# Kernel optimization log

Hardware: AMD Instinct MI355X
Metric: run time of the kernel (lower is better)

The kernel has to match this reference:

```python
import jax, jax.numpy as jnp
import numpy as np

N_NODES = 100000
N_EDGES = 600000
N_GRAPHS = 512
VOCAB = 4096
EMB = 128
HID = 128


def setup_inputs() -> dict:
    key = jax.random.key(0)
    ks = jax.random.split(key, 8)
    x = jax.random.randint(ks[0], (N_NODES,), 0, VOCAB)
    edge_index = jax.random.randint(ks[1], (2, N_EDGES), 0, N_NODES)
    batch = jnp.sort(jax.random.randint(ks[2], (N_NODES,), 0, N_GRAPHS))
    emb = jax.random.normal(ks[3], (VOCAB, EMB), dtype=jnp.float32)
    W1 = jax.random.normal(ks[4], (EMB, HID), dtype=jnp.float32) / np.sqrt(EMB)
    b1 = jnp.zeros((HID,), dtype=jnp.float32)
    W2 = jax.random.normal(ks[5], (HID, HID), dtype=jnp.float32) / np.sqrt(HID)
    b2 = jnp.zeros((HID,), dtype=jnp.float32)
    return {"x": x, "edge_index": edge_index, "batch": batch,
            "emb": emb, "W1": W1, "b1": b1, "W2": W2, "b2": b2}


def gcn_conv(h, src, dst, W, b, n_nodes):
    # PyG GCNConv: linear transform, then symmetric-normalized scatter-sum
    # (self-loops already included in src/dst), plus bias.
    h = h @ W
    deg = jax.ops.segment_sum(jnp.ones(dst.shape, h.dtype), dst, num_segments=n_nodes)
    dis = jnp.where(deg > 0, jax.lax.rsqrt(jnp.maximum(deg, 1.0)), 0.0)
    norm = dis[src] * dis[dst]                      # [E]
    msg = h[src] * norm[:, None]                    # gather + scale
    out = jax.ops.segment_sum(msg, dst, num_segments=n_nodes)
    return out + b


def reference(x, edge_index, batch, emb, W1, b1, W2, b2):
    n = x.shape[0]
    loop = jnp.arange(n)
    src = jnp.concatenate([edge_index[0], loop])    # add self-loops, as GCNConv does
    dst = jnp.concatenate([edge_index[1], loop])

    h = emb[x]                                      # [N, EMB] embedding lookup
    h = jax.nn.relu(gcn_conv(h, src, dst, W1, b1, n))
    # dropout: identity in eval mode
    h = gcn_conv(h, src, dst, W2, b2, n)            # [N, HID]

    # global_mean_pool over graph ids
    sums = jax.ops.segment_sum(h, batch, num_segments=N_GRAPHS)
    cnts = jax.ops.segment_sum(jnp.ones((n,), h.dtype), batch, num_segments=N_GRAPHS)
    return sums / jnp.maximum(cnts, 1.0)[:, None]   # [N_GRAPHS, HID]
```

## Files before the change

### kernel.cpp

```cpp
#include <hip/hip_runtime.h>
#include <hip/hip_bf16.h>
#include <hip/hip_fp16.h>

#define D 128

__device__ __forceinline__ float bf2f(unsigned short u) {
  return __uint_as_float(((unsigned int)u) << 16);
}
__device__ __forceinline__ unsigned short f2bf(float f) {
  unsigned int x = __float_as_uint(f);
  x += 0x7fff + ((x >> 16) & 1);
  return (unsigned short)(x >> 16);
}
__device__ __forceinline__ float h2f(unsigned short b) {
  return __half2float(__ushort_as_half(b));
}


__global__ void k_detect_f5(const unsigned short* __restrict__ t0, int n0,
                            const unsigned short* __restrict__ t1, int n1,
                            const unsigned short* __restrict__ t2, int n2,
                            const unsigned short* __restrict__ t3, int n3,
                            const unsigned short* __restrict__ t4, int n4,
                            int* __restrict__ flag) {
  const unsigned short* tabs[5] = {t0, t1, t2, t3, t4};
  int ns[5] = {n0, n1, n2, n3, n4};
  int b = blockIdx.x;
  const unsigned short* u16 = tabs[b];
  int n = ns[b];
  __shared__ int cnt;
  int K = n / 2 < 256 ? n / 2 : 256;
  if (threadIdx.x == 0) cnt = 0;
  __syncthreads();
  if (threadIdx.x < K) {
    unsigned short u = u16[threadIdx.x * 2];
    int e = (u >> 7) & 0xFF;
    if (u == 0 || (e >= 100 && e <= 140)) atomicAdd(&cnt, 1);
  }
  __syncthreads();
  if (threadIdx.x == 0) flag[b] = (cnt * 2 >= K) ? 1 : 0;
}

__global__ void k_detect_i(const unsigned int* __restrict__ ei32,
                           int* __restrict__ flagSlot) {
  __shared__ int z;
  if (threadIdx.x == 0) z = 0;
  __syncthreads();
  if (ei32[threadIdx.x * 2 + 1] == 0u) atomicAdd(&z, 1);
  __syncthreads();
  if (threadIdx.x == 0) *flagSlot = (z >= 60) ? 1 : 0;
}

__global__ void k_conv(const void* __restrict__ src, float* __restrict__ dst,
                       int n, const int* __restrict__ flagSlot) {
  int i = blockIdx.x * blockDim.x + threadIdx.x;
  if (i >= n) return;
  if (*flagSlot) dst[i] = bf2f(((const unsigned short*)src)[i]);
  else           dst[i] = ((const float*)src)[i];
}

__global__ void k_conv_params(const void* __restrict__ W1, const void* __restrict__ b1,
                              const void* __restrict__ W2, const void* __restrict__ b2,
                              float* __restrict__ W1f, float* __restrict__ b1f,
                              float* __restrict__ W2f, float* __restrict__ b2f,
                              const int* __restrict__ flag) {
  int i = blockIdx.x * blockDim.x + threadIdx.x;
  const int S = D * D;
  const void* src; float* dst; int j; const int* fs;
  if (i < S)                { src = W1; dst = W1f; j = i;            fs = flag + 1; }
  else if (i < S + D)       { src = b1; dst = b1f; j = i - S;        fs = flag + 2; }
  else if (i < 2 * S + D)   { src = W2; dst = W2f; j = i - S - D;    fs = flag + 3; }
  else if (i < 2 * S + 2*D) { src = b2; dst = b2f; j = i - 2*S - D;  fs = flag + 4; }
  else return;
  if (*fs) dst[j] = bf2f(((const unsigned short*)src)[j]);
  else     dst[j] = ((const float*)src)[j];
}

__global__ void k_convi_all(const void* __restrict__ xr, const void* __restrict__ eir,
                            const void* __restrict__ br,
                            int* __restrict__ xs, int* __restrict__ srcs,
                            int* __restrict__ dsts, int* __restrict__ batchs,
                            int* __restrict__ indeg,
                            int nn, int ne, int vocab, int ng,
                            const int* __restrict__ flag64) {
  long long i = (long long)blockIdx.x * blockDim.x + threadIdx.x;
  int is64 = *flag64;
  if (i < nn) {
    int v = is64 ? (int)((const long long*)xr)[i] : ((const int*)xr)[i];
    v = v < 0 ? 0 : (v > vocab - 1 ? vocab - 1 : v);
    xs[i] = v;
  } else if (i < (long long)nn + ne) {
    long long j = i - nn;
    int v = is64 ? (int)((const long long*)eir)[j] : ((const int*)eir)[j];
    v = v < 0 ? 0 : (v > nn - 1 ? nn - 1 : v);
    srcs[j] = v;
  } else if (i < (long long)nn + 2 * ne) {
    long long j = i - nn - ne;
    int v = is64 ? (int)((const long long*)eir)[ne + j] : ((const int*)eir)[ne + j];
    v = v < 0 ? 0 : (v > nn - 1 ? nn - 1 : v);
    dsts[j] = v;
    atomicAdd(&indeg[v], 1);
  } else if (i < 2LL * nn + 2 * ne) {
    long long j = i - nn - 2 * ne;
    int v = is64 ? (int)((const long long*)br)[j] : ((const int*)br)[j];
    v = v < 0 ? 0 : (v > ng - 1 ? ng - 1 : v);
    batchs[j] = v;
  }
}

__global__ __launch_bounds__(1024) void k_scan1(const int* __restrict__ indeg,
                                                int* __restrict__ off,
                                                int* __restrict__ bsum, int nn) {
  int t = threadIdx.x;
  int idx = blockIdx.x * 1024 + t;
  int v = (idx < nn) ? indeg[idx] : 0;
  int lane = t & 63, wid = t >> 6;
  int inc = v;
  #pragma unroll
  for (int d = 1; d < 64; d <<= 1) {
    int u = __shfl_up(inc, d);
    if (lane >= d) inc += u;
  }
  __shared__ int ws[16];
  if (lane == 63) ws[wid] = inc;
  __syncthreads();
  if (wid == 0) {
    int wv = (lane < 16) ? ws[lane] : 0;
    #pragma unroll
    for (int d = 1; d < 16; d <<= 1) {
      int u = __shfl_up(wv, d);
      if (lane >= d) wv += u;
    }
    if (lane < 16) ws[lane] = wv;
  }
  __syncthreads();
  int base = wid ? ws[wid - 1] : 0;
  if (idx < nn) off[idx] = base + inc - v;
  if (t == 1023) bsum[blockIdx.x] = ws[15];
}

__global__ void k_scan2(int* __restrict__ bsum, int nb) {
  if (blockIdx.x == 0 && threadIdx.x == 0) {
    int run = 0;
    for (int i = 0; i < nb; ++i) { int s = bsum[i]; bsum[i] = run; run += s; }
  }
}

__global__ void k_scan3(int* __restrict__ off, int* __restrict__ cursor,
                        float* __restrict__ dis, const int* __restrict__ indeg,
                        const int* __restrict__ bsum, int nn) {
  int idx = blockIdx.x * blockDim.x + threadIdx.x;
  if (idx >= nn) return;
  int o = off[idx] + bsum[idx >> 10];
  off[idx] = o;
  cursor[idx] = o;
  dis[idx] = rsqrtf((float)indeg[idx] + 1.0f);
}

__global__ void k_fill(const int* __restrict__ srcA, const int* __restrict__ dstA,
                       const int* __restrict__ xs, const float* __restrict__ dis,
                       int* __restrict__ cursor, int2* __restrict__ csr, int ne) {
  int e = blockIdx.x * blockDim.x + threadIdx.x;
  if (e >= ne) return;
  int d = dstA[e], s = srcA[e];
  unsigned short hb = __half_as_ushort(__float2half_rn(dis[s]));
  unsigned int packed = (unsigned int)xs[s] | ((unsigned int)hb << 16);
  int pp = atomicAdd(&cursor[d], 1);
  csr[pp] = make_int2(s, (int)packed);
}

__global__ void k_gemm_dumb(const float* __restrict__ A,
                            const float* __restrict__ W,
                            float* __restrict__ OUT, int rows) {
  int idx = blockIdx.x * blockDim.x + threadIdx.x;
  if (idx >= rows * D) return;
  int r = idx >> 7, c = idx & 127;
  const float* a = A + (size_t)r * D;
  float acc = 0.f;
  for (int k = 0; k < D; ++k) acc += a[k] * W[k * D + c];
  OUT[idx] = acc;
}

__global__ __launch_bounds__(256) void k_aggrelu(const int* __restrict__ x,
                                                 const float* __restrict__ G,
                                                 const float* __restrict__ b1,
                                                 const int* __restrict__ off,
                                                 const int* __restrict__ indeg,
                                                 const float* __restrict__ dis,
                                                 const int2* __restrict__ csr,
                                                 unsigned short* __restrict__ H1,
                                                 int nn) {
  int gid = blockIdx.x * blockDim.x + threadIdx.x;
  int n = gid >> 5;
  if (n >= nn) return;
  int lane = threadIdx.x & 31;
  float dn = dis[n];
  float4 g0 = ((const float4*)(G + (size_t)x[n] * D))[lane];
  float ax = dn * g0.x, ay = dn * g0.y, az = dn * g0.z, aw = dn * g0.w;
  int s0 = off[n], m = indeg[n];
  if (m >= 2) {
    unsigned int c0 = (unsigned int)csr[s0].y, c1 = (unsigned int)csr[s0 + 1].y;
    int j = 0;
    for (; j + 3 < m; j += 2) {
      unsigned int p0 = (unsigned int)csr[s0 + j + 2].y;
      unsigned int p1 = (unsigned int)csr[s0 + j + 3].y;
      float w0 = h2f((unsigned short)(c0 >> 16));
      float w1 = h2f((unsigned short)(c1 >> 16));
      float4 gA = ((const float4*)(G + (size_t)(c0 & 0xFFFF) * D))[lane];
      float4 gB = ((const float4*)(G + (size_t)(c1 & 0xFFFF) * D))[lane];
      ax += w0 * gA.x + w1 * gB.x;
      ay += w0 * gA.y + w1 * gB.y;
      az += w0 * gA.z + w1 * gB.z;
      aw += w0 * gA.w + w1 * gB.w;
      c0 = p0; c1 = p1;
    }
    {
      float w0 = h2f((unsigned short)(c0 >> 16));
      float w1 = h2f((unsigned short)(c1 >> 16));
      float4 gA = ((const float4*)(G + (size_t)(c0 & 0xFFFF) * D))[lane];
      float4 gB = ((const float4*)(G + (size_t)(c1 & 0xFFFF) * D))[lane];
      ax += w0 * gA.x + w1 * gB.x;
      ay += w0 * gA.y + w1 * gB.y;
      az += w0 * gA.z + w1 * gB.z;
      aw += w0 * gA.w + w1 * gB.w;
    }
    if (j + 2 < m) {
      unsigned int e0 = (unsigned int)csr[s0 + j + 2].y;
      float w0 = h2f((unsigned short)(e0 >> 16));
      float4 gA = ((const float4*)(G + (size_t)(e0 & 0xFFFF) * D))[lane];
      ax += w0 * gA.x; ay += w0 * gA.y; az += w0 * gA.z; aw += w0 * gA.w;
    }
  } else if (m == 1) {
    unsigned int e0 = (unsigned int)csr[s0].y;
    float w0 = h2f((unsigned short)(e0 >> 16));
    float4 gA = ((const float4*)(G + (size_t)(e0 & 0xFFFF) * D))[lane];
    ax += w0 * gA.x; ay += w0 * gA.y; az += w0 * gA.z; aw += w0 * gA.w;
  }
  float4 bb = ((const float4*)b1)[lane];
  ushort4 o;
  o.x = f2bf(dn * fmaxf(dn * ax + bb.x, 0.f));
  o.y = f2bf(dn * fmaxf(dn * ay + bb.y, 0.f));
  o.z = f2bf(dn * fmaxf(dn * az + bb.z, 0.f));
  o.w = f2bf(dn * fmaxf(dn * aw + bb.w, 0.f));
  ((ushort4*)(H1 + (size_t)n * D))[lane] = o;
}

__global__ __launch_bounds__(256) void k_agg2pool(
    const unsigned short* __restrict__ H1, const int* __restrict__ off,
    const int* __restrict__ indeg, const float* __restrict__ dis,
    const int2* __restrict__ csr, const int* __restrict__ batch,
    float* __restrict__ P, int nn) {
  __shared__ float buf[8][D];
  __shared__ int gbuf[8];
  int t = threadIdx.x;
  int slot = t >> 5, lane = t & 31;
  int n = blockIdx.x * 8 + slot;
  float ax = 0.f, ay = 0.f, az = 0.f, aw = 0.f;
  if (n < nn) {
    float dn = dis[n];
    ushort4 u0 = ((const ushort4*)(H1 + (size_t)n * D))[lane];
    ax = bf2f(u0.x); ay = bf2f(u0.y); az = bf2f(u0.z); aw = bf2f(u0.w);
    int s0 = off[n], m = indeg[n];
    if (m >= 2) {
      int c0 = csr[s0].x, c1 = csr[s0 + 1].x;
      int j = 0;
      for (; j + 3 < m; j += 2) {
        int p0 = csr[s0 + j + 2].x;
        int p1 = csr[s0 + j + 3].x;
        ushort4 hA = ((const ushort4*)(H1 + (size_t)c0 * D))[lane];
        ushort4 hB = ((const ushort4*)(H1 + (size_t)c1 * D))[lane];
        ax += bf2f(hA.x) + bf2f(hB.x);
        ay += bf2f(hA.y) + bf2f(hB.y);
        az += bf2f(hA.z) + bf2f(hB.z);
        aw += bf2f(hA.w) + bf2f(hB.w);
        c0 = p0; c1 = p1;
      }
      {
        ushort4 hA = ((const ushort4*)(H1 + (size_t)c0 * D))[lane];
        ushort4 hB = ((const ushort4*)(H1 + (size_t)c1 * D))[lane];
        ax += bf2f(hA.x) + bf2f(hB.x);
        ay += bf2f(hA.y) + bf2f(hB.y);
        az += bf2f(hA.z) + bf2f(hB.z);
        aw += bf2f(hA.w) + bf2f(hB.w);
      }
      if (j + 2 < m) {
        int e0 = csr[s0 + j + 2].x;
        ushort4 hA = ((const ushort4*)(H1 + (size_t)e0 * D))[lane];
        ax += bf2f(hA.x); ay += bf2f(hA.y); az += bf2f(hA.z); aw += bf2f(hA.w);
      }
    } else if (m == 1) {
      int e0 = csr[s0].x;
      ushort4 hA = ((const ushort4*)(H1 + (size_t)e0 * D))[lane];
      ax += bf2f(hA.x); ay += bf2f(hA.y); az += bf2f(hA.z); aw += bf2f(hA.w);
    }
    ax *= dn; ay *= dn; az *= dn; aw *= dn;
  }
  ((float4*)&buf[slot][lane * 4])[0] = make_float4(ax, ay, az, aw);
  if (lane == 0) gbuf[slot] = (n < nn) ? batch[n] : -1;
  __syncthreads();
  if (t < D) {
    int c = t;
    float acc = 0.f;
    int run = -1;
    #pragma unroll
    for (int s2 = 0; s2 < 8; ++s2) {
      int g = gbuf[s2];
      if (g < 0) break;
      if (g != run) {
        if (run >= 0) atomicAdd(&P[(size_t)run * D + c], acc);
        run = g;
        acc = 0.f;
      }
      acc += buf[s2][c];
    }
    if (run >= 0) atomicAdd(&P[(size_t)run * D + c], acc);
  }
}

__global__ void k_cnt2(const int* __restrict__ batch, int* __restrict__ cnt,
                       int nn, int ng) {
  int g = blockIdx.x * blockDim.x + threadIdx.x;
  if (g >= ng) return;
  int lo = 0, hi = nn;
  while (lo < hi) { int m = (lo + hi) >> 1; if (batch[m] < g) lo = m + 1; else hi = m; }
  int s = lo;
  hi = nn;
  while (lo < hi) { int m = (lo + hi) >> 1; if (batch[m] < g + 1) lo = m + 1; else hi = m; }
  cnt[g] = lo - s;
}

__global__ void k_out_dumb(const float* __restrict__ P,
                           const int* __restrict__ cnt,
                           const float* __restrict__ W2,
                           const float* __restrict__ b2,
                           float* __restrict__ Out, int ng) {
  int idx = blockIdx.x * blockDim.x + threadIdx.x;
  if (idx >= ng * D) return;
  int g = idx >> 7, c = idx & 127;
  int m = cnt[g];
  float inv = (m > 0) ? (1.0f / (float)m) : 0.0f;
  const float* pr = P + (size_t)g * D;
  float acc = 0.f;
  for (int k = 0; k < D; ++k) acc += pr[k] * W2[k * D + c];
  acc *= inv;
  if (m > 0) acc += b2[c];
  Out[idx] = acc;
}

extern "C" void kernel_launch(void* const* d_in, const int* in_sizes, int n_in,
                              void* d_out, int out_size, void* d_ws, size_t ws_size,
                              hipStream_t stream) {
  const void* xr = d_in[0];
  const void* eir = d_in[1];
  const void* batchr = d_in[2];
  const void* emb = d_in[3];
  const void* W1 = d_in[4];
  const void* b1 = d_in[5];
  const void* W2 = d_in[6];
  const void* b2 = d_in[7];
  float* out = (float*)d_out;

  const int nn = in_sizes[0];
  const int ne = in_sizes[1] / 2;
  const int vocab = in_sizes[3] / D;
  const int ng = out_size / D;
  const int nb = (nn + 1023) / 1024;

  char* p = (char*)d_ws;
  auto alloc = [&](size_t bytes) -> char* {
    char* r = p;
    p += (bytes + 511) & ~(size_t)511;
    return r;
  };
  int* flag = (int*)alloc(512);
  int* xs = (int*)alloc((size_t)nn * 4);
  int* srcs = (int*)alloc((size_t)ne * 4);
  int* dsts = (int*)alloc((size_t)ne * 4);
  int* batchs = (int*)alloc((size_t)nn * 4);
  int* indeg = (int*)alloc((size_t)nn * 4);
  int* off = (int*)alloc((size_t)nn * 4);
  int* cursor = (int*)alloc((size_t)nn * 4);
  float* dis = (float*)alloc((size_t)nn * 4);
  int* bsum = (int*)alloc((size_t)nb * 4);
  int* cnt = (int*)alloc((size_t)ng * 4);
  int2* csr = (int2*)alloc((size_t)ne * 8);
  float* embf = (float*)alloc((size_t)vocab * D * 4);
  float* W1f = (float*)alloc((size_t)D * D * 4);
  float* b1f = (float*)alloc((size_t)D * 4);
  float* W2f = (float*)alloc((size_t)D * D * 4);
  float* b2f = (float*)alloc((size_t)D * 4);
  float* G = (float*)alloc((size_t)vocab * D * 4);
  unsigned short* H1 = (unsigned short*)alloc((size_t)nn * D * 2);
  float* P = (float*)alloc((size_t)ng * D * 4);

  hipMemsetAsync(flag, 0, 512, stream);
  hipMemsetAsync(indeg, 0, (size_t)nn * 4, stream);
  hipMemsetAsync(P, 0, (size_t)ng * D * 4, stream);

  k_detect_f5<<<5, 256, 0, stream>>>(
      (const unsigned short*)emb, vocab * D,
      (const unsigned short*)W1, D * D,
      (const unsigned short*)b1, D,
      (const unsigned short*)W2, D * D,
      (const unsigned short*)b2, D, flag);
  k_detect_i<<<1, 64, 0, stream>>>((const unsigned int*)eir, flag + 5);

  k_conv<<<(vocab * D + 255) / 256, 256, 0, stream>>>(emb, embf, vocab * D, flag + 0);
  k_conv_params<<<(2 * D * D + 2 * D + 255) / 256, 256, 0, stream>>>(
      W1, b1, W2, b2, W1f, b1f, W2f, b2f, flag);

  {
    long long tot = 2LL * nn + 2LL * ne;
    k_convi_all<<<(int)((tot + 255) / 256), 256, 0, stream>>>(
        xr, eir, batchr, xs, srcs, dsts, batchs, indeg, nn, ne, vocab, ng, flag + 5);
  }

  k_scan1<<<nb, 1024, 0, stream>>>(indeg, off, bsum, nn);
  k_scan2<<<1, 64, 0, stream>>>(bsum, nb);
  k_scan3<<<(nn + 255) / 256, 256, 0, stream>>>(off, cursor, dis, indeg, bsum, nn);
  k_fill<<<(ne + 255) / 256, 256, 0, stream>>>(srcs, dsts, xs, dis, cursor, csr, ne);

  k_gemm_dumb<<<(vocab * D + 255) / 256, 256, 0, stream>>>(embf, W1f, G, vocab);

  {
    long long thr = (long long)nn * 32;
    k_aggrelu<<<(int)((thr + 255) / 256), 256, 0, stream>>>(xs, G, b1f, off, indeg,
                                                            dis, csr, H1, nn);
  }
  k_agg2pool<<<(nn + 7) / 8, 256, 0, stream>>>(H1, off, indeg, dis, csr,
                                               batchs, P, nn);
  k_cnt2<<<(ng + 255) / 256, 256, 0, stream>>>(batchs, cnt, nn, ng);
  k_out_dumb<<<(ng * D + 255) / 256, 256, 0, stream>>>(P, cnt, W2f, b2f, out, ng);
}
```

Baseline: 249.5 us.

## Fuse prep kernels, fold dtype conversion into consumers, widen aggregation to 64 lanes

Merges the detection kernels and the memsets into one prep kernel, and fuses scan2 with scan3 so each block computes its own prefix from bsum. Removes the separate dtype-conversion kernels by converting bf16 inline inside the GEMM, the aggregation and the output kernels, and folds the count kernel into the output kernel. Changes both aggregation kernels from 32 to 64 lanes per node with float2/ushort2 loads and 4-way unrolled edge loops. The goal is fewer launches and narrower per-lane gathers. In exchange, each output thread repeats the binary searches, and the flag branches add per-thread checks.

Result: slower. 263.2 us (+5.5%).

```diff
diff --git a/kernel.cpp b/kernel.cpp
--- a/kernel.cpp
+++ b/kernel.cpp
@@ -17,63 +17,44 @@
 }
 
 
-__global__ void k_detect_f5(const unsigned short* __restrict__ t0, int n0,
-                            const unsigned short* __restrict__ t1, int n1,
-                            const unsigned short* __restrict__ t2, int n2,
-                            const unsigned short* __restrict__ t3, int n3,
-                            const unsigned short* __restrict__ t4, int n4,
-                            int* __restrict__ flag) {
-  const unsigned short* tabs[5] = {t0, t1, t2, t3, t4};
-  int ns[5] = {n0, n1, n2, n3, n4};
+__global__ void k_prep(const unsigned short* __restrict__ t0, int n0,
+                       const unsigned short* __restrict__ t1, int n1,
+                       const unsigned short* __restrict__ t2, int n2,
+                       const unsigned short* __restrict__ t3, int n3,
+                       const unsigned short* __restrict__ t4, int n4,
+                       const unsigned int* __restrict__ ei32,
+                       int* __restrict__ flag, int* __restrict__ indeg,
+                       float* __restrict__ P, int nn, int ngD) {
   int b = blockIdx.x;
-  const unsigned short* u16 = tabs[b];
-  int n = ns[b];
-  __shared__ int cnt;
-  int K = n / 2 < 256 ? n / 2 : 256;
-  if (threadIdx.x == 0) cnt = 0;
-  __syncthreads();
-  if (threadIdx.x < K) {
-    unsigned short u = u16[threadIdx.x * 2];
-    int e = (u >> 7) & 0xFF;
-    if (u == 0 || (e >= 100 && e <= 140)) atomicAdd(&cnt, 1);
-  }
-  __syncthreads();
-  if (threadIdx.x == 0) flag[b] = (cnt * 2 >= K) ? 1 : 0;
-}
-
-__global__ void k_detect_i(const unsigned int* __restrict__ ei32,
-                           int* __restrict__ flagSlot) {
-  __shared__ int z;
-  if (threadIdx.x == 0) z = 0;
-  __syncthreads();
-  if (ei32[threadIdx.x * 2 + 1] == 0u) atomicAdd(&z, 1);
-  __syncthreads();
-  if (threadIdx.x == 0) *flagSlot = (z >= 60) ? 1 : 0;
-}
-
-__global__ void k_conv(const void* __restrict__ src, float* __restrict__ dst,
-                       int n, const int* __restrict__ flagSlot) {
-  int i = blockIdx.x * blockDim.x + threadIdx.x;
-  if (i >= n) return;
-  if (*flagSlot) dst[i] = bf2f(((const unsigned short*)src)[i]);
-  else           dst[i] = ((const float*)src)[i];
-}
-
-__global__ void k_conv_params(const void* __restrict__ W1, const void* __restrict__ b1,
-                              const void* __restrict__ W2, const void* __restrict__ b2,
-                              float* __restrict__ W1f, float* __restrict__ b1f,
-                              float* __restrict__ W2f, float* __restrict__ b2f,
-                              const int* __restrict__ flag) {
-  int i = blockIdx.x * blockDim.x + threadIdx.x;
-  const int S = D * D;
-  const void* src; float* dst; int j; const int* fs;
-  if (i < S)                { src = W1; dst = W1f; j = i;            fs = flag + 1; }
-  else if (i < S + D)       { src = b1; dst = b1f; j = i - S;        fs = flag + 2; }
-  else if (i < 2 * S + D)   { src = W2; dst = W2f; j = i - S - D;    fs = flag + 3; }
-  else if (i < 2 * S + 2*D) { src = b2; dst = b2f; j = i - 2*S - D;  fs = flag + 4; }
-  else return;
-  if (*fs) dst[j] = bf2f(((const unsigned short*)src)[j]);
-  else     dst[j] = ((const float*)src)[j];
+  if (b < 5) {
+    const unsigned short* tabs[5] = {t0, t1, t2, t3, t4};
+    int ns[5] = {n0, n1, n2, n3, n4};
+    const unsigned short* u16 = tabs[b];
+    int n = ns[b];
+    __shared__ int cnt;
+    int K = n / 2 < 256 ? n / 2 : 256;
+    if (threadIdx.x == 0) cnt = 0;
+    __syncthreads();
+    if (threadIdx.x < K) {
+      unsigned short u = u16[threadIdx.x * 2];
+      int e = (u >> 7) & 0xFF;
+      if (u == 0 || (e >= 100 && e <= 140)) atomicAdd(&cnt, 1);
+    }
+    __syncthreads();
+    if (threadIdx.x == 0) flag[b] = (cnt * 2 >= K) ? 1 : 0;
+  } else if (b == 5) {
+    __shared__ int z;
+    if (threadIdx.x == 0) z = 0;
+    __syncthreads();
+    if (threadIdx.x < 64 && ei32[threadIdx.x * 2 + 1] == 0u) atomicAdd(&z, 1);
+    __syncthreads();
+    if (threadIdx.x == 0) flag[5] = (z >= 60) ? 1 : 0;
+  } else {
+    int i = (b - 6) * 256 + threadIdx.x;
+    if (i < nn) indeg[i] = 0;
+    int j = i - nn;
+    if (j >= 0 && j < ngD) P[j] = 0.f;
+  }
 }
 
 __global__ void k_convi_all(const void* __restrict__ xr, const void* __restrict__ eir,
@@ -139,22 +120,35 @@
   if (t == 1023) bsum[blockIdx.x] = ws[15];
 }
 
-__global__ void k_scan2(int* __restrict__ bsum, int nb) {
-  if (blockIdx.x == 0 && threadIdx.x == 0) {
-    int run = 0;
-    for (int i = 0; i < nb; ++i) { int s = bsum[i]; bsum[i] = run; run += s; }
-  }
-}
-
-__global__ void k_scan3(int* __restrict__ off, int* __restrict__ cursor,
-                        float* __restrict__ dis, const int* __restrict__ indeg,
-                        const int* __restrict__ bsum, int nn) {
-  int idx = blockIdx.x * blockDim.x + threadIdx.x;
-  if (idx >= nn) return;
-  int o = off[idx] + bsum[idx >> 10];
-  off[idx] = o;
-  cursor[idx] = o;
-  dis[idx] = rsqrtf((float)indeg[idx] + 1.0f);
+__global__ __launch_bounds__(1024) void k_scan23(int* __restrict__ off,
+                                                 int* __restrict__ cursor,
+                                                 float* __restrict__ dis,
+                                                 const int* __restrict__ indeg,
+                                                 const int* __restrict__ bsum,
+                                                 int nn) {
+  int b = blockIdx.x, t = threadIdx.x;
+  int v = (t < b) ? bsum[t] : 0;
+  #pragma unroll
+  for (int d = 32; d; d >>= 1) v += __shfl_xor(v, d);
+  __shared__ int ws[16];
+  __shared__ int prefix;
+  int lane = t & 63, wid = t >> 6;
+  if (lane == 0) ws[wid] = v;
+  __syncthreads();
+  if (t == 0) {
+    int s = 0;
+    #pragma unroll
+    for (int i = 0; i < 16; ++i) s += ws[i];
+    prefix = s;
+  }
+  __syncthreads();
+  int idx = b * 1024 + t;
+  if (idx < nn) {
+    int o = off[idx] + prefix;
+    off[idx] = o;
+    cursor[idx] = o;
+    dis[idx] = rsqrtf((float)indeg[idx] + 1.0f);
+  }
 }
 
 __global__ void k_fill(const int* __restrict__ srcA, const int* __restrict__ dstA,
@@ -169,83 +163,84 @@
   csr[pp] = make_int2(s, (int)packed);
 }
 
-__global__ void k_gemm_dumb(const float* __restrict__ A,
-                            const float* __restrict__ W,
-                            float* __restrict__ OUT, int rows) {
+__global__ void k_gemm(const void* __restrict__ emb, const void* __restrict__ W1,
+                       float* __restrict__ G, int vocab,
+                       const int* __restrict__ flag) {
   int idx = blockIdx.x * blockDim.x + threadIdx.x;
-  if (idx >= rows * D) return;
+  if (idx >= vocab * D) return;
   int r = idx >> 7, c = idx & 127;
-  const float* a = A + (size_t)r * D;
+  int fe = flag[0], fw = flag[1];
+  const float* ef = (const float*)emb;
+  const unsigned short* eu = (const unsigned short*)emb;
+  const float* wf = (const float*)W1;
+  const unsigned short* wu = (const unsigned short*)W1;
+  size_t ro = (size_t)r * D;
   float acc = 0.f;
-  for (int k = 0; k < D; ++k) acc += a[k] * W[k * D + c];
-  OUT[idx] = acc;
+  if (fe) {
+    if (fw) { for (int k = 0; k < D; ++k) acc += bf2f(eu[ro + k]) * bf2f(wu[k * D + c]); }
+    else    { for (int k = 0; k < D; ++k) acc += bf2f(eu[ro + k]) * wf[k * D + c]; }
+  } else {
+    if (fw) { for (int k = 0; k < D; ++k) acc += ef[ro + k] * bf2f(wu[k * D + c]); }
+    else    { for (int k = 0; k < D; ++k) acc += ef[ro + k] * wf[k * D + c]; }
+  }
+  G[idx] = acc;
 }
 
 __global__ __launch_bounds__(256) void k_aggrelu(const int* __restrict__ x,
                                                  const float* __restrict__ G,
-                                                 const float* __restrict__ b1,
+                                                 const void* __restrict__ b1,
                                                  const int* __restrict__ off,
                                                  const int* __restrict__ indeg,
                                                  const float* __restrict__ dis,
                                                  const int2* __restrict__ csr,
                                                  unsigned short* __restrict__ H1,
-                                                 int nn) {
+                                                 int nn, const int* __restrict__ flag) {
   int gid = blockIdx.x * blockDim.x + threadIdx.x;
-  int n = gid >> 5;
+  int n = gid >> 6;
   if (n >= nn) return;
-  int lane = threadIdx.x & 31;
+  int lane = threadIdx.x & 63;
   float dn = dis[n];
-  float4 g0 = ((const float4*)(G + (size_t)x[n] * D))[lane];
-  float ax = dn * g0.x, ay = dn * g0.y, az = dn * g0.z, aw = dn * g0.w;
+  const float2* G2 = (const float2*)G;
+  float2 g0 = G2[(size_t)x[n] * 64 + lane];
+  float ax = dn * g0.x, ay = dn * g0.y;
   int s0 = off[n], m = indeg[n];
-  if (m >= 2) {
-    unsigned int c0 = (unsigned int)csr[s0].y, c1 = (unsigned int)csr[s0 + 1].y;
-    int j = 0;
-    for (; j + 3 < m; j += 2) {
-      unsigned int p0 = (unsigned int)csr[s0 + j + 2].y;
-      unsigned int p1 = (unsigned int)csr[s0 + j + 3].y;
-      float w0 = h2f((unsigned short)(c0 >> 16));
-      float w1 = h2f((unsigned short)(c1 >> 16));
-      float4 gA = ((const float4*)(G + (size_t)(c0 & 0xFFFF) * D))[lane];
-      float4 gB = ((const float4*)(G + (size_t)(c1 & 0xFFFF) * D))[lane];
-      ax += w0 * gA.x + w1 * gB.x;
-      ay += w0 * gA.y + w1 * gB.y;
-      az += w0 * gA.z + w1 * gB.z;
-      aw += w0 * gA.w + w1 * gB.w;
-      c0 = p0; c1 = p1;
-    }
-    {
-      float w0 = h2f((unsigned short)(c0 >> 16));
-      float w1 = h2f((unsigned short)(c1 >> 16));
-      float4 gA = ((const float4*)(G + (size_t)(c0 & 0xFFFF) * D))[lane];
-      float4 gB = ((const float4*)(G + (size_t)(c1 & 0xFFFF) * D))[lane];
-      ax += w0 * gA.x + w1 * gB.x;
-      ay += w0 * gA.y + w1 * gB.y;
-      az += w0 * gA.z + w1 * gB.z;
-      aw += w0 * gA.w + w1 * gB.w;
-    }
-    if (j + 2 < m) {
-      unsigned int e0 = (unsigned int)csr[s0 + j + 2].y;
-      float w0 = h2f((unsigned short)(e0 >> 16));
-      float4 gA = ((const float4*)(G + (size_t)(e0 & 0xFFFF) * D))[lane];
-      ax += w0 * gA.x; ay += w0 * gA.y; az += w0 * gA.z; aw += w0 * gA.w;
-    }
-  } else if (m == 1) {
-    unsigned int e0 = (unsigned int)csr[s0].y;
-    float w0 = h2f((unsigned short)(e0 >> 16));
-    float4 gA = ((const float4*)(G + (size_t)(e0 & 0xFFFF) * D))[lane];
-    ax += w0 * gA.x; ay += w0 * gA.y; az += w0 * gA.z; aw += w0 * gA.w;
-  }
-  float4 bb = ((const float4*)b1)[lane];
-  ushort4 o;
-  o.x = f2bf(dn * fmaxf(dn * ax + bb.x, 0.f));
-  o.y = f2bf(dn * fmaxf(dn * ay + bb.y, 0.f));
-  o.z = f2bf(dn * fmaxf(dn * az + bb.z, 0.f));
-  o.w = f2bf(dn * fmaxf(dn * aw + bb.w, 0.f));
-  ((ushort4*)(H1 + (size_t)n * D))[lane] = o;
-}
-
-__global__ __launch_bounds__(256) void k_agg2pool(
+  int j = 0;
+  for (; j + 4 <= m; j += 4) {
+    unsigned c0 = (unsigned)csr[s0 + j].y, c1 = (unsigned)csr[s0 + j + 1].y;
+    unsigned c2 = (unsigned)csr[s0 + j + 2].y, c3 = (unsigned)csr[s0 + j + 3].y;
+    float w0 = h2f((unsigned short)(c0 >> 16));
+    float w1 = h2f((unsigned short)(c1 >> 16));
+    float w2 = h2f((unsigned short)(c2 >> 16));
+    float w3 = h2f((unsigned short)(c3 >> 16));
+    float2 gA = G2[(size_t)(c0 & 0xFFFFu) * 64 + lane];
+    float2 gB = G2[(size_t)(c1 & 0xFFFFu) * 64 + lane];
+    float2 gC = G2[(size_t)(c2 & 0xFFFFu) * 64 + lane];
+    float2 gD = G2[(size_t)(c3 & 0xFFFFu) * 64 + lane];
+    ax += w0 * gA.x + w1 * gB.x + w2 * gC.x + w3 * gD.x;
+    ay += w0 * gA.y + w1 * gB.y + w2 * gC.y + w3 * gD.y;
+  }
+  for (; j < m; ++j) {
+    unsigned c = (unsigned)csr[s0 + j].y;
+    float w = h2f((unsigned short)(c >> 16));
+    float2 g = G2[(size_t)(c & 0xFFFFu) * 64 + lane];
+    ax += w * g.x;
+    ay += w * g.y;
+  }
+  float bx, by;
+  if (flag[2]) {
+    const unsigned short* bu = (const unsigned short*)b1;
+    bx = bf2f(bu[2 * lane]); by = bf2f(bu[2 * lane + 1]);
+  } else {
+    float2 bb = ((const float2*)b1)[lane];
+    bx = bb.x; by = bb.y;
+  }
+  ushort2 o;
+  o.x = f2bf(dn * fmaxf(dn * ax + bx, 0.f));
+  o.y = f2bf(dn * fmaxf(dn * ay + by, 0.f));
+  ((ushort2*)(H1 + (size_t)n * D))[lane] = o;
+}
+
+__global__ __launch_bounds__(512) void k_agg2pool(
     const unsigned short* __restrict__ H1, const int* __restrict__ off,
     const int* __restrict__ indeg, const float* __restrict__ dis,
     const int2* __restrict__ csr, const int* __restrict__ batch,
@@ -253,49 +248,34 @@
   __shared__ float buf[8][D];
   __shared__ int gbuf[8];
   int t = threadIdx.x;
-  int slot = t >> 5, lane = t & 31;
+  int slot = t >> 6, lane = t & 63;
   int n = blockIdx.x * 8 + slot;
-  float ax = 0.f, ay = 0.f, az = 0.f, aw = 0.f;
+  float ax = 0.f, ay = 0.f;
   if (n < nn) {
     float dn = dis[n];
-    ushort4 u0 = ((const ushort4*)(H1 + (size_t)n * D))[lane];
-    ax = bf2f(u0.x); ay = bf2f(u0.y); az = bf2f(u0.z); aw = bf2f(u0.w);
+    const ushort2* H2 = (const ushort2*)H1;
+    ushort2 u0 = H2[(size_t)n * 64 + lane];
+    ax = bf2f(u0.x); ay = bf2f(u0.y);
     int s0 = off[n], m = indeg[n];
-    if (m >= 2) {
-      int c0 = csr[s0].x, c1 = csr[s0 + 1].x;
-      int j = 0;
-      for (; j + 3 < m; j += 2) {
-        int p0 = csr[s0 + j + 2].x;
-        int p1 = csr[s0 + j + 3].x;
-        ushort4 hA = ((const ushort4*)(H1 + (size_t)c0 * D))[lane];
-        ushort4 hB = ((const ushort4*)(H1 + (size_t)c1 * D))[lane];
-        ax += bf2f(hA.x) + bf2f(hB.x);
-        ay += bf2f(hA.y) + bf2f(hB.y);
-        az += bf2f(hA.z) + bf2f(hB.z);
-        aw += bf2f(hA.w) + bf2f(hB.w);
-        c0 = p0; c1 = p1;
-      }
-      {
-        ushort4 hA = ((const ushort4*)(H1 + (size_t)c0 * D))[lane];
-        ushort4 hB = ((const ushort4*)(H1 + (size_t)c1 * D))[lane];
-        ax += bf2f(hA.x) + bf2f(hB.x);
-        ay += bf2f(hA.y) + bf2f(hB.y);
-        az += bf2f(hA.z) + bf2f(hB.z);
-        aw += bf2f(hA.w) + bf2f(hB.w);
-      }
-      if (j + 2 < m) {
-        int e0 = csr[s0 + j + 2].x;
-        ushort4 hA = ((const ushort4*)(H1 + (size_t)e0 * D))[lane];
-        ax += bf2f(hA.x); ay += bf2f(hA.y); az += bf2f(hA.z); aw += bf2f(hA.w);
-      }
-    } else if (m == 1) {
-      int e0 = csr[s0].x;
-      ushort4 hA = ((const ushort4*)(H1 + (size_t)e0 * D))[lane];
-      ax += bf2f(hA.x); ay += bf2f(hA.y); az += bf2f(hA.z); aw += bf2f(hA.w);
+    int j = 0;
+    for (; j + 4 <= m; j += 4) {
+      int e0 = csr[s0 + j].x, e1 = csr[s0 + j + 1].x;
+      int e2 = csr[s0 + j + 2].x, e3 = csr[s0 + j + 3].x;
+      ushort2 hA = H2[(size_t)e0 * 64 + lane];
+      ushort2 hB = H2[(size_t)e1 * 64 + lane];
+      ushort2 hC = H2[(size_t)e2 * 64 + lane];
+      ushort2 hD = H2[(size_t)e3 * 64 + lane];
+      ax += bf2f(hA.x) + bf2f(hB.x) + bf2f(hC.x) + bf2f(hD.x);
+      ay += bf2f(hA.y) + bf2f(hB.y) + bf2f(hC.y) + bf2f(hD.y);
     }
-    ax *= dn; ay *= dn; az *= dn; aw *= dn;
-  }
-  ((float4*)&buf[slot][lane * 4])[0] = make_float4(ax, ay, az, aw);
+    for (; j < m; ++j) {
+      int e = csr[s0 + j].x;
+      ushort2 h = H2[(size_t)e * 64 + lane];
+      ax += bf2f(h.x); ay += bf2f(h.y);
+    }
+    ax *= dn; ay *= dn;
+  }
+  ((float2*)&buf[slot][2 * lane])[0] = make_float2(ax, ay);
   if (lane == 0) gbuf[slot] = (n < nn) ? batch[n] : -1;
   __syncthreads();
   if (t < D) {
@@ -317,33 +297,31 @@
   }
 }
 
-__global__ void k_cnt2(const int* __restrict__ batch, int* __restrict__ cnt,
-                       int nn, int ng) {
-  int g = blockIdx.x * blockDim.x + threadIdx.x;
-  if (g >= ng) return;
-  int lo = 0, hi = nn;
-  while (lo < hi) { int m = (lo + hi) >> 1; if (batch[m] < g) lo = m + 1; else hi = m; }
-  int s = lo;
-  hi = nn;
-  while (lo < hi) { int m = (lo + hi) >> 1; if (batch[m] < g + 1) lo = m + 1; else hi = m; }
-  cnt[g] = lo - s;
-}
-
-__global__ void k_out_dumb(const float* __restrict__ P,
-                           const int* __restrict__ cnt,
-                           const float* __restrict__ W2,
-                           const float* __restrict__ b2,
-                           float* __restrict__ Out, int ng) {
+__global__ void k_out(const float* __restrict__ P, const int* __restrict__ batch,
+                      const void* __restrict__ W2, const void* __restrict__ b2,
+                      float* __restrict__ Out, int ng, int nn,
+                      const int* __restrict__ flag) {
   int idx = blockIdx.x * blockDim.x + threadIdx.x;
   if (idx >= ng * D) return;
   int g = idx >> 7, c = idx & 127;
-  int m = cnt[g];
+  int lo = 0, hi = nn;
+  while (lo < hi) { int mid = (lo + hi) >> 1; if (batch[mid] < g) lo = mid + 1; else hi = mid; }
+  int s = lo;
+  hi = nn;
+  while (lo < hi) { int mid = (lo + hi) >> 1; if (batch[mid] < g + 1) lo = mid + 1; else hi = mid; }
+  int m = lo - s;
   float inv = (m > 0) ? (1.0f / (float)m) : 0.0f;
   const float* pr = P + (size_t)g * D;
   float acc = 0.f;
-  for (int k = 0; k < D; ++k) acc += pr[k] * W2[k * D + c];
+  if (flag[3]) {
+    const unsigned short* wu = (const unsigned short*)W2;
+    for (int k = 0; k < D; ++k) acc += pr[k] * bf2f(wu[k * D + c]);
+  } else {
+    const float* wf = (const float*)W2;
+    for (int k = 0; k < D; ++k) acc += pr[k] * wf[k * D + c];
+  }
   acc *= inv;
-  if (m > 0) acc += b2[c];
+  if (m > 0) acc += flag[4] ? bf2f(((const unsigned short*)b2)[c]) : ((const float*)b2)[c];
   Out[idx] = acc;
 }
 
@@ -365,6 +343,7 @@
   const int vocab = in_sizes[3] / D;
   const int ng = out_size / D;
   const int nb = (nn + 1023) / 1024;
+  const int ngD = ng * D;
 
   char* p = (char*)d_ws;
   auto alloc = [&](size_t bytes) -> char* {
@@ -382,32 +361,21 @@
   int* cursor = (int*)alloc((size_t)nn * 4);
   float* dis = (float*)alloc((size_t)nn * 4);
   int* bsum = (int*)alloc((size_t)nb * 4);
-  int* cnt = (int*)alloc((size_t)ng * 4);
   int2* csr = (int2*)alloc((size_t)ne * 8);
-  float* embf = (float*)alloc((size_t)vocab * D * 4);
-  float* W1f = (float*)alloc((size_t)D * D * 4);
-  float* b1f = (float*)alloc((size_t)D * 4);
-  float* W2f = (float*)alloc((size_t)D * D * 4);
-  float* b2f = (float*)alloc((size_t)D * 4);
   float* G = (float*)alloc((size_t)vocab * D * 4);
   unsigned short* H1 = (unsigned short*)alloc((size_t)nn * D * 2);
-  float* P = (float*)alloc((size_t)ng * D * 4);
-
-  hipMemsetAsync(flag, 0, 512, stream);
-  hipMemsetAsync(indeg, 0, (size_t)nn * 4, stream);
-  hipMemsetAsync(P, 0, (size_t)ng * D * 4, stream);
-
-  k_detect_f5<<<5, 256, 0, stream>>>(
-      (const unsigned short*)emb, vocab * D,
-      (const unsigned short*)W1, D * D,
-      (const unsigned short*)b1, D,
-      (const unsigned short*)W2, D * D,
-      (const unsigned short*)b2, D, flag);
-  k_detect_i<<<1, 64, 0, stream>>>((const unsigned int*)eir, flag + 5);
-
-  k_conv<<<(vocab * D + 255) / 256, 256, 0, stream>>>(emb, embf, vocab * D, flag + 0);
-  k_conv_params<<<(2 * D * D + 2 * D + 255) / 256, 256, 0, stream>>>(
-      W1, b1, W2, b2, W1f, b1f, W2f, b2f, flag);
+  float* P = (float*)alloc((size_t)ngD * 4);
+
+  {
+    int zb = (nn + ngD + 255) / 256;
+    k_prep<<<6 + zb, 256, 0, stream>>>(
+        (const unsigned short*)emb, vocab * D,
+        (const unsigned short*)W1, D * D,
+        (const unsigned short*)b1, D,
+        (const unsigned short*)W2, D * D,
+        (const unsigned short*)b2, D,
+        (const unsigned int*)eir, flag, indeg, P, nn, ngD);
+  }
 
   {
     long long tot = 2LL * nn + 2LL * ne;
@@ -416,19 +384,19 @@
   }
 
   k_scan1<<<nb, 1024, 0, stream>>>(indeg, off, bsum, nn);
-  k_scan2<<<1, 64, 0, stream>>>(bsum, nb);
-  k_scan3<<<(nn + 255) / 256, 256, 0, stream>>>(off, cursor, dis, indeg, bsum, nn);
+  k_scan23<<<nb, 1024, 0, stream>>>(off, cursor, dis, indeg, bsum, nn);
   k_fill<<<(ne + 255) / 256, 256, 0, stream>>>(srcs, dsts, xs, dis, cursor, csr, ne);
 
-  k_gemm_dumb<<<(vocab * D + 255) / 256, 256, 0, stream>>>(embf, W1f, G, vocab);
+  k_gemm<<<(vocab * D + 255) / 256, 256, 0, stream>>>(emb, W1, G, vocab, flag);
 
   {
-    long long thr = (long long)nn * 32;
-    k_aggrelu<<<(int)((thr + 255) / 256), 256, 0, stream>>>(xs, G, b1f, off, indeg,
-                                                            dis, csr, H1, nn);
-  }
-  k_agg2pool<<<(nn + 7) / 8, 256, 0, stream>>>(H1, off, indeg, dis, csr,
+    long long thr = (long long)nn * 64;
+    k_aggrelu<<<(int)((thr + 255) / 256), 256, 0, stream>>>(xs, G, b1, off, indeg,
+                                                            dis, csr, H1, nn, flag);
+  }
+
+  k_agg2pool<<<(nn + 7) / 8, 512, 0, stream>>>(H1, off, indeg, dis, csr,
                                                batchs, P, nn);
-  k_cnt2<<<(ng + 255) / 256, 256, 0, stream>>>(batchs, cnt, nn, ng);
-  k_out_dumb<<<(ng * D + 255) / 256, 256, 0, stream>>>(P, cnt, W2f, b2f, out, ng);
-}
+
+  k_out<<<(ngD + 255) / 256, 256, 0, stream>>>(P, batchs, W2, b2, out, ng, nn, flag);
+}
```
